# Performance work log

Hardware: AMD Instinct MI355X
Metric: run time of the kernel (lower is better)

The kernel has to match this reference:

```python
import jax, jax.numpy as jnp
import numpy as np

B, N, DIN, DH = 16, 512, 128, 256
NEG = -9.0e15  # matches -9000000000000000.0 in torch source


def _xavier(key, fan_in, fan_out):
    lim = float(np.sqrt(6.0 / (fan_in + fan_out)))
    return jax.random.uniform(key, (fan_in, fan_out), jnp.float32, -lim, lim)


def _l2n(x, eps=1e-12):
    # torch F.normalize: x / max(||x||, eps)
    return x / jnp.maximum(jnp.linalg.norm(x, axis=-1, keepdims=True), eps)


def _prelu(x, a):
    return jnp.where(x >= 0, x, a * x)


def setup_inputs() -> dict:
    key = jax.random.key(0)
    ks = jax.random.split(key, 12)
    seq = jax.random.normal(ks[0], (B, N, DIN), jnp.float32)
    # sparse-ish nonnegative adjacency with self loops, row-normalized
    u = jax.random.uniform(ks[1], (B, N, N), jnp.float32)
    a = jnp.where(u < 0.1, u, 0.0) + jnp.eye(N, dtype=jnp.float32)[None]
    adj = a / a.sum(-1, keepdims=True)
    # dense diffusion matrix, row-normalized
    d = jax.random.uniform(ks[2], (B, N, N), jnp.float32)
    diff = d / d.sum(-1, keepdims=True)
    # dropout keep-mask for F.dropout(p=0.1, training=True)
    keep = jax.random.bernoulli(ks[3], 0.9, (B, N, N)).astype(jnp.float32)
    drop_mask = keep / 0.9
    return {
        "seq": seq, "adj": adj, "diff": diff, "drop_mask": drop_mask,
        "fc1_w": _xavier(ks[4], DIN, DH),
        "q_w": _xavier(ks[5], DH, DH),
        "k_w": _xavier(ks[6], DH, DH),
        "v_w1": _xavier(ks[7], DH, DH),
        "v_w2": _xavier(ks[8], DH, DH),
        "fc2_w": _xavier(ks[9], DIN, DH),
        "bias1": jnp.zeros((DH,), jnp.float32),
        "bias2": jnp.zeros((DH,), jnp.float32),
        "prelu1_a": jnp.float32(0.25),
        "prelu2_a": jnp.float32(0.25),
        "v_prelu_a": jnp.float32(0.25),
    }


def reference(seq, adj, diff, drop_mask, fc1_w, q_w, k_w, v_w1, v_w2,
              fc2_w, bias1, bias2, prelu1_a, prelu2_a, v_prelu_a):
    # ---- GCN1 (attention branch) ----
    fts = seq @ fc1_w                                   # [B,N,H]
    out = jnp.einsum('bmn,bnh->bmh', adj, fts)          # adj aggregation
    q = _l2n(out @ q_w)
    k = _l2n(out @ k_w)
    scores = jax.lax.stop_gradient(jnp.einsum('bmd,bnd->bmn', q, k))  # .detach()
    div_loss = jnp.mean(jnp.sum((q - k) ** 2, axis=-1))
    att = jnp.where(adj > 0, scores, NEG)
    att = jax.nn.softmax(att, axis=-1) * drop_mask      # dropout(p=0.1)
    agg = jnp.einsum('bmn,bnh->bmh', att, out)
    v = _prelu(agg @ v_w1, v_prelu_a) @ v_w2 + bias1
    h1 = _prelu(v, prelu1_a)
    # ---- GCN2 (plain branch) ----
    h2 = _prelu(jnp.einsum('bmn,bnh->bmh', diff, seq @ fc2_w) + bias2, prelu2_a)
    # ---- Readout ----
    c1 = jnp.mean(h1, axis=1)                           # [B,H]
    c2 = jnp.mean(h2, axis=1)
    # ---- DIS ----
    n1 = _l2n(h1).reshape(B * N, DH)
    n2 = _l2n(h2).reshape(B * N, DH)
    node_logits = n1 @ n2.T                             # [B*N, B*N]
    graph_logits = _l2n(c1) @ _l2n(c2).T                # [B, B]
    return node_logits, graph_logits, div_loss
```

## Files before the change

kernel.cpp:

```cpp
#include <hip/hip_runtime.h>
#include <hip/hip_bf16.h>


using bf16x8 = __attribute__((ext_vector_type(8))) short;
using f32x4  = __attribute__((ext_vector_type(4))) float;

__device__ __forceinline__ unsigned short f2b(float f) {
    union { float f; unsigned int u; } x; x.f = f;
    unsigned int r = x.u + 0x7FFFu + ((x.u >> 16) & 1u);
    return (unsigned short)(r >> 16);
}
__device__ __forceinline__ float b2f(unsigned short u) {
    union { unsigned int u; float f; } x; x.u = (unsigned int)u << 16;
    return x.f;
}
__device__ __forceinline__ void gload_lds16(const void* g, void* l) {
    __builtin_amdgcn_global_load_lds(
        (const __attribute__((address_space(1))) void*)g,
        (__attribute__((address_space(3))) void*)l, 16, 0, 0);
}

__global__ __launch_bounds__(256) void conv3(const float* __restrict__ seq,
                                             const float* __restrict__ adj,
                                             const float* __restrict__ diff,
                                             unsigned short* __restrict__ seq_bf,
                                             unsigned short* __restrict__ adj_bf,
                                             unsigned short* __restrict__ diff_bf) {
    long i = (long)blockIdx.x * 256 + threadIdx.x;
    const float* src; unsigned short* dst; long off;
    if (i < 262144)       { src = seq;  dst = seq_bf;  off = i; }
    else if (i < 1310720) { src = adj;  dst = adj_bf;  off = i - 262144; }
    else                  { src = diff; dst = diff_bf; off = i - 1310720; }
    float4 v = reinterpret_cast<const float4*>(src)[off];
    ushort4 o; o.x = f2b(v.x); o.y = f2b(v.y); o.z = f2b(v.z); o.w = f2b(v.w);
    reinterpret_cast<ushort4*>(dst)[off] = o;
}

__global__ void wtrans6(const float* __restrict__ fc1, const float* __restrict__ fc2,
                        const float* __restrict__ qw,  const float* __restrict__ kw,
                        const float* __restrict__ v1,  const float* __restrict__ v2,
                        unsigned short* fc1T, unsigned short* fc2T,
                        unsigned short* qwT,  unsigned short* kwT,
                        unsigned short* v1T,  unsigned short* v2T) {
    __shared__ float t[32][33];
    const int z = blockIdx.z;
    const float* in; unsigned short* op; int R;
    const int C = 256;
    if      (z == 0) { in = fc1; op = fc1T; R = 128; }
    else if (z == 1) { in = fc2; op = fc2T; R = 128; }
    else if (z == 2) { in = qw;  op = qwT;  R = 256; }
    else if (z == 3) { in = kw;  op = kwT;  R = 256; }
    else if (z == 4) { in = v1;  op = v1T;  R = 256; }
    else             { in = v2;  op = v2T;  R = 256; }
    int c0 = blockIdx.x * 32, r0 = blockIdx.y * 32;
    if (r0 >= R) return;
    int x = threadIdx.x, y = threadIdx.y;
    for (int i = 0; i < 32; i += 8) t[y + i][x] = in[(long)(r0 + y + i) * C + c0 + x];
    __syncthreads();
    for (int i = 0; i < 32; i += 8)
        op[(long)(c0 + y + i) * R + r0 + x] = f2b(t[x][y + i]);
}

#define BN 128
#define BK 64

template<int TBM, int EPI, bool WF, bool WB, bool WT, bool SWZ>
__global__ __launch_bounds__(256) void gemm_nt(
    const unsigned short* __restrict__ A, const unsigned short* __restrict__ Bt,
    float* __restrict__ Cf, unsigned short* __restrict__ Cb, unsigned short* __restrict__ Ct,
    int M, int Nn, int K, int lda, int ldb, int ldc, int ldt,
    long sA, long sB, long sC, long sT,
    const float* __restrict__ bias, const float* __restrict__ alpha_ptr)
{
    constexpr int MI = TBM / 32;
    __shared__ unsigned short As[TBM][BK];
    __shared__ unsigned short Bs[BN][BK];
    const int b = blockIdx.z;
    A  += (long)b * sA;
    Bt += (long)b * sB;
    const long cbase = (long)b * sC;
    const long tbase = (long)b * sT;

    int tx, ty;
    if (SWZ) {
        int bid = blockIdx.y * gridDim.x + blockIdx.x;
        int nwg = gridDim.x * gridDim.y;
        int cpx = nwg >> 3;
        int s = (bid & 7) * cpx + (bid >> 3);
        tx = s % gridDim.x; ty = s / gridDim.x;
    } else { tx = blockIdx.x; ty = blockIdx.y; }
    const int tile_m = ty * TBM;
    const int tile_n = tx * BN;

    const int tid  = threadIdx.x;
    const int lane = tid & 63;
    const int wave = tid >> 6;
    const int wm = (wave >> 1) * (TBM / 2);
    const int wn = (wave & 1) << 6;
    const int lrow = lane >> 3;
    const int lcol = (lane & 7) << 3;

    f32x4 acc[MI][4] = {};

    for (int k0 = 0; k0 < K; k0 += BK) {
        #pragma unroll
        for (int i = 0; i < TBM / 32; ++i) {
            const int rb = (i * 4 + wave) * 8;
            gload_lds16(A + (long)(tile_m + rb + lrow) * lda + k0 + lcol, &As[rb][0]);
        }
        #pragma unroll
        for (int i = 0; i < 4; ++i) {
            const int rb = (i * 4 + wave) * 8;
            gload_lds16(Bt + (long)(tile_n + rb + lrow) * ldb + k0 + lcol, &Bs[rb][0]);
        }
        __syncthreads();
        #pragma unroll
        for (int ks = 0; ks < 2; ++ks) {
            const int kk = ks * 32 + ((lane >> 4) << 3);
            bf16x8 af[MI], bq[4];
            #pragma unroll
            for (int mi = 0; mi < MI; ++mi)
                af[mi] = *reinterpret_cast<const bf16x8*>(&As[wm + (lane & 15) + mi * 16][kk]);
            #pragma unroll
            for (int ni = 0; ni < 4; ++ni)
                bq[ni] = *reinterpret_cast<const bf16x8*>(&Bs[wn + (lane & 15) + ni * 16][kk]);
            #pragma unroll
            for (int mi = 0; mi < MI; ++mi)
                #pragma unroll
                for (int ni = 0; ni < 4; ++ni)
                    acc[mi][ni] = __builtin_amdgcn_mfma_f32_16x16x32_bf16(
                        af[mi], bq[ni], acc[mi][ni], 0, 0, 0);
        }
        __syncthreads();
    }

    const float alpha = (EPI & 1) ? alpha_ptr[0] : 0.f;
    const int c0 = lane & 15;
    const int r0 = (lane >> 4) << 2;
    #pragma unroll
    for (int ni = 0; ni < 4; ++ni) {
        const int col = tile_n + wn + ni * 16 + c0;
        const float bv = (EPI & 2) ? bias[col] : 0.f;
        #pragma unroll
        for (int mi = 0; mi < MI; ++mi) {
            const int row0 = tile_m + wm + mi * 16 + r0;
            float v[4];
            #pragma unroll
            for (int j = 0; j < 4; ++j) {
                float x = acc[mi][ni][j] + bv;
                if (EPI & 1) x = (x >= 0.f) ? x : alpha * x;
                v[j] = x;
            }
            if (WF) {
                #pragma unroll
                for (int j = 0; j < 4; ++j)
                    Cf[cbase + (long)(row0 + j) * ldc + col] = v[j];
            }
            if (WB) {
                #pragma unroll
                for (int j = 0; j < 4; ++j)
                    Cb[cbase + (long)(row0 + j) * ldc + col] = f2b(v[j]);
            }
            if (WT) {
                ushort4 o; o.x = f2b(v[0]); o.y = f2b(v[1]); o.z = f2b(v[2]); o.w = f2b(v[3]);
                *reinterpret_cast<ushort4*>(&Ct[tbase + (long)col * ldt + row0]) = o;
            }
        }
    }
}

__global__ __launch_bounds__(256) void gemm_norm(
    const unsigned short* __restrict__ A, const unsigned short* __restrict__ Bt,
    unsigned short* __restrict__ n_out, float* __restrict__ psum,
    const float* __restrict__ bias, const float* __restrict__ alpha_ptr,
    int K, int lda, int ldb, long sA, long sB)
{
    __shared__ unsigned short As[32][BK];
    __shared__ unsigned short Bs[256][BK];
    __shared__ float rowred[32][4];
    A  += (long)blockIdx.z * sA;
    Bt += (long)blockIdx.z * sB;
    const int p = blockIdx.z * gridDim.y + blockIdx.y;
    const int arow0 = blockIdx.y * 32;
    const long grow0 = (long)p * 32;

    const int tid  = threadIdx.x;
    const int lane = tid & 63;
    const int wave = tid >> 6;
    const int wn = wave << 6;
    const int lrow = lane >> 3;
    const int lcol = (lane & 7) << 3;

    f32x4 acc[2][4] = {};

    for (int k0 = 0; k0 < K; k0 += BK) {
        {
            const int rb = wave * 8;
            gload_lds16(A + (long)(arow0 + rb + lrow) * lda + k0 + lcol, &As[rb][0]);
        }
        #pragma unroll
        for (int i = 0; i < 8; ++i) {
            const int rb = (i * 4 + wave) * 8;
            gload_lds16(Bt + (long)(rb + lrow) * ldb + k0 + lcol, &Bs[rb][0]);
        }
        __syncthreads();
        #pragma unroll
        for (int ks = 0; ks < 2; ++ks) {
            const int kk = ks * 32 + ((lane >> 4) << 3);
            bf16x8 af[2], bq[4];
            #pragma unroll
            for (int mi = 0; mi < 2; ++mi)
                af[mi] = *reinterpret_cast<const bf16x8*>(&As[(lane & 15) + mi * 16][kk]);
            #pragma unroll
            for (int ni = 0; ni < 4; ++ni)
                bq[ni] = *reinterpret_cast<const bf16x8*>(&Bs[wn + (lane & 15) + ni * 16][kk]);
            #pragma unroll
            for (int mi = 0; mi < 2; ++mi)
                #pragma unroll
                for (int ni = 0; ni < 4; ++ni)
                    acc[mi][ni] = __builtin_amdgcn_mfma_f32_16x16x32_bf16(
                        af[mi], bq[ni], acc[mi][ni], 0, 0, 0);
        }
        __syncthreads();
    }

    const float alpha = alpha_ptr[0];
    const int c0 = lane & 15;
    const int r0 = (lane >> 4) << 2;
    float rs[2][4] = {};
    #pragma unroll
    for (int ni = 0; ni < 4; ++ni) {
        const float bv = bias[wn + ni * 16 + c0];
        #pragma unroll
        for (int mi = 0; mi < 2; ++mi)
            #pragma unroll
            for (int j = 0; j < 4; ++j) {
                float x = acc[mi][ni][j] + bv;
                x = (x >= 0.f) ? x : alpha * x;
                acc[mi][ni][j] = x;
                rs[mi][j] += x * x;
            }
    }
    #pragma unroll
    for (int o = 1; o <= 8; o <<= 1)
        #pragma unroll
        for (int mi = 0; mi < 2; ++mi)
            #pragma unroll
            for (int j = 0; j < 4; ++j) rs[mi][j] += __shfl_xor(rs[mi][j], o);
    if ((lane & 15) == 0) {
        #pragma unroll
        for (int mi = 0; mi < 2; ++mi)
            #pragma unroll
            for (int j = 0; j < 4; ++j) rowred[mi * 16 + r0 + j][wave] = rs[mi][j];
    }
    __syncthreads();
    float inv[2][4];
    #pragma unroll
    for (int mi = 0; mi < 2; ++mi)
        #pragma unroll
        for (int j = 0; j < 4; ++j) {
            const int r = mi * 16 + r0 + j;
            float s = rowred[r][0] + rowred[r][1] + rowred[r][2] + rowred[r][3];
            inv[mi][j] = 1.f / fmaxf(sqrtf(s), 1e-12f);
        }
    float cs[4];
    #pragma unroll
    for (int ni = 0; ni < 4; ++ni) {
        float s = 0.f;
        #pragma unroll
        for (int mi = 0; mi < 2; ++mi)
            #pragma unroll
            for (int j = 0; j < 4; ++j) s += acc[mi][ni][j];
        s += __shfl_xor(s, 16);
        s += __shfl_xor(s, 32);
        cs[ni] = s;
    }
    if (lane < 16) {
        #pragma unroll
        for (int ni = 0; ni < 4; ++ni)
            psum[(long)p * 256 + wn + ni * 16 + lane] = cs[ni];
    }
    #pragma unroll
    for (int ni = 0; ni < 4; ++ni)
        #pragma unroll
        for (int mi = 0; mi < 2; ++mi)
            #pragma unroll
            for (int j = 0; j < 4; ++j)
                n_out[(grow0 + mi * 16 + r0 + j) * 256 + wn + ni * 16 + c0] =
                    f2b(acc[mi][ni][j] * inv[mi][j]);
}

__global__ __launch_bounds__(256) void qk_post(const float* __restrict__ qk,
                                               unsigned short* __restrict__ q_bf,
                                               unsigned short* __restrict__ k_bf,
                                               float* __restrict__ rowpart) {
    long row = blockIdx.x; int t = threadIdx.x;
    float v = qk[row * 512 + t];
    float w = qk[row * 512 + 256 + t];
    float sq = v * v, sk = w * w;
    #pragma unroll
    for (int o = 32; o; o >>= 1) { sq += __shfl_xor(sq, o); sk += __shfl_xor(sk, o); }
    __shared__ float rq[4], rk[4], rd[4];
    if ((t & 63) == 0) { rq[t >> 6] = sq; rk[t >> 6] = sk; }
    __syncthreads();
    sq = rq[0] + rq[1] + rq[2] + rq[3];
    sk = rk[0] + rk[1] + rk[2] + rk[3];
    float qn = v / fmaxf(sqrtf(sq), 1e-12f);
    float kn = w / fmaxf(sqrtf(sk), 1e-12f);
    q_bf[row * 256 + t] = f2b(qn);
    k_bf[row * 256 + t] = f2b(kn);
    float d = qn - kn, sd = d * d;
    #pragma unroll
    for (int o = 32; o; o >>= 1) sd += __shfl_xor(sd, o);
    if ((t & 63) == 0) rd[t >> 6] = sd;
    __syncthreads();
    if (t == 0) rowpart[row] = rd[0] + rd[1] + rd[2] + rd[3];
}

__global__ __launch_bounds__(256) void att_softmax(const unsigned short* __restrict__ scores,
                                                   const unsigned short* __restrict__ adj_bf,
                                                   const float* __restrict__ drop,
                                                   unsigned short* __restrict__ att) {
    long base = ((long)blockIdx.y * 512 + blockIdx.x) * 512;
    int t = threadIdx.x;
    unsigned short a0 = adj_bf[base + t], a1 = adj_bf[base + t + 256];
    float s0 = b2f(scores[base + t]), s1 = b2f(scores[base + t + 256]);
    bool m0 = a0 != 0, m1 = a1 != 0;
    float mx = fmaxf(m0 ? s0 : -1e30f, m1 ? s1 : -1e30f);
    #pragma unroll
    for (int o = 32; o; o >>= 1) mx = fmaxf(mx, __shfl_xor(mx, o));
    __shared__ float redm[4], reds[4];
    if ((t & 63) == 0) redm[t >> 6] = mx;
    __syncthreads();
    mx = fmaxf(fmaxf(redm[0], redm[1]), fmaxf(redm[2], redm[3]));
    float e0 = m0 ? __expf(s0 - mx) : 0.f;
    float e1 = m1 ? __expf(s1 - mx) : 0.f;
    float sm = e0 + e1;
    #pragma unroll
    for (int o = 32; o; o >>= 1) sm += __shfl_xor(sm, o);
    if ((t & 63) == 0) reds[t >> 6] = sm;
    __syncthreads();
    sm = reds[0] + reds[1] + reds[2] + reds[3];
    float inv = 1.f / sm;
    att[base + t]       = f2b(e0 * inv * drop[base + t]);
    att[base + t + 256] = f2b(e1 * inv * drop[base + t + 256]);
}

__global__ __launch_bounds__(256) void graphf2(const float* __restrict__ psum1,
                                               const float* __restrict__ psum2,
                                               const float* __restrict__ rowpart,
                                               float* __restrict__ out_g,
                                               float* __restrict__ out_div) {
    __shared__ float a[16][256], bsm[16][256];
    int t = threadIdx.x, g = t >> 4, l = t & 15;
    float va[16], vb[16]; float s1 = 0.f, s2 = 0.f;
    #pragma unroll
    for (int i = 0; i < 16; ++i) {
        const int col = l + i * 16;
        float m1 = 0.f, m2 = 0.f;
        for (int c = 0; c < 16; ++c) {
            m1 += psum1[(long)(g * 16 + c) * 256 + col];
            m2 += psum2[(long)(g * 16 + c) * 256 + col];
        }
        va[i] = m1 * (1.f / 512.f); s1 += va[i] * va[i];
        vb[i] = m2 * (1.f / 512.f); s2 += vb[i] * vb[i];
    }
    #pragma unroll
    for (int o = 8; o; o >>= 1) { s1 += __shfl_xor(s1, o, 16); s2 += __shfl_xor(s2, o, 16); }
    float d1 = fmaxf(sqrtf(s1), 1e-12f), d2 = fmaxf(sqrtf(s2), 1e-12f);
    #pragma unroll
    for (int i = 0; i < 16; ++i) {
        a[g][l + i * 16] = va[i] / d1;
        bsm[g][l + i * 16] = vb[i] / d2;
    }
    __syncthreads();
    int ii = t >> 4, jj = t & 15;
    float s = 0.f;
    for (int h = 0; h < 256; ++h) s += a[ii][h] * bsm[jj][h];
    out_g[ii * 16 + jj] = s;
    float ds = 0.f;
    for (int i = t; i < 8192; i += 256) ds += rowpart[i];
    #pragma unroll
    for (int o = 32; o; o >>= 1) ds += __shfl_xor(ds, o);
    __shared__ float red[4];
    if ((t & 63) == 0) red[t >> 6] = ds;
    __syncthreads();
    if (t == 0) out_div[0] = (red[0] + red[1] + red[2] + red[3]) * (1.f / 8192.f);
}

static constexpr long OFF_SEQ_BF  = 0;
static constexpr long OFF_FC1T    = 2097152;
static constexpr long OFF_FC2T    = OFF_FC1T + 65536;
static constexpr long OFF_QWT     = OFF_FC2T + 65536;
static constexpr long OFF_KWT     = OFF_QWT + 131072;
static constexpr long OFF_VW1T    = OFF_KWT + 131072;
static constexpr long OFF_VW2T    = OFF_VW1T + 131072;
static constexpr long OFF_ROWPART = OFF_VW2T + 131072;
static constexpr long OFF_ADJATT  = 3145728;
static constexpr long OFF_DIFFBF  = OFF_ADJATT + 8388608;
static constexpr long OFF_FTST    = OFF_DIFFBF + 8388608;
static constexpr long OFF_OUTT    = OFF_FTST + 4194304;
static constexpr long OFF_QF      = OFF_OUTT + 4194304;
static constexpr long OFF_QBF     = OFF_QF + 16777216;
static constexpr long OFF_KBF     = OFF_QBF + 4194304;
static constexpr long OFF_SCORES  = OFF_KBF + 4194304;

extern "C" void kernel_launch(void* const* d_in, const int* in_sizes, int n_in,
                              void* d_out, int out_size, void* d_ws, size_t ws_size,
                              hipStream_t stream) {
    const float* seq      = (const float*)d_in[0];
    const float* adj      = (const float*)d_in[1];
    const float* diff     = (const float*)d_in[2];
    const float* drop     = (const float*)d_in[3];
    const float* fc1_w    = (const float*)d_in[4];
    const float* q_w      = (const float*)d_in[5];
    const float* k_w      = (const float*)d_in[6];
    const float* v_w1     = (const float*)d_in[7];
    const float* v_w2     = (const float*)d_in[8];
    const float* fc2_w    = (const float*)d_in[9];
    const float* bias1    = (const float*)d_in[10];
    const float* bias2    = (const float*)d_in[11];
    const float* prelu1_a = (const float*)d_in[12];
    const float* prelu2_a = (const float*)d_in[13];
    const float* v_prelu  = (const float*)d_in[14];
    float* out = (float*)d_out;

    char* ws = (char*)d_ws;
    unsigned short* seq_bf  = (unsigned short*)(ws + OFF_SEQ_BF);
    unsigned short* fc1T    = (unsigned short*)(ws + OFF_FC1T);
    unsigned short* fc2T    = (unsigned short*)(ws + OFF_FC2T);
    unsigned short* qwT     = (unsigned short*)(ws + OFF_QWT);
    unsigned short* kwT     = (unsigned short*)(ws + OFF_KWT);
    unsigned short* vw1T    = (unsigned short*)(ws + OFF_VW1T);
    unsigned short* vw2T    = (unsigned short*)(ws + OFF_VW2T);
    float*          rowpart = (float*)(ws + OFF_ROWPART);
    unsigned short* adj_bf  = (unsigned short*)(ws + OFF_ADJATT);
    unsigned short* att_bf  = (unsigned short*)(ws + OFF_ADJATT);
    unsigned short* diff_bf = (unsigned short*)(ws + OFF_DIFFBF);
    unsigned short* ftsT    = (unsigned short*)(ws + OFF_FTST);
    unsigned short* outT    = (unsigned short*)(ws + OFF_OUTT);
    float*          qk_f    = (float*)(ws + OFF_QF);
    float*          psum1   = (float*)(ws + OFF_QF);
    float*          psum2   = (float*)(ws + OFF_QF + 262144);
    unsigned short* q_bf    = (unsigned short*)(ws + OFF_QBF);
    unsigned short* agg_bf  = (unsigned short*)(ws + OFF_QBF);
    unsigned short* fts2T   = (unsigned short*)(ws + OFF_QBF);
    unsigned short* k_bf    = (unsigned short*)(ws + OFF_KBF);
    unsigned short* t1_bf   = (unsigned short*)(ws + OFF_KBF);
    unsigned short* out_bf  = (unsigned short*)(ws + OFF_SCORES);
    unsigned short* scoresb = (unsigned short*)(ws + OFF_SCORES);
    unsigned short* n1_bf   = (unsigned short*)(ws + OFF_SCORES);
    unsigned short* n2_bf   = (unsigned short*)(ws + OFF_SCORES + 4194304);

    conv3<<<9216, 256, 0, stream>>>(seq, adj, diff, seq_bf, adj_bf, diff_bf);
    wtrans6<<<dim3(8, 8, 6), dim3(32, 8), 0, stream>>>(
        fc1_w, fc2_w, q_w, k_w, v_w1, v_w2, fc1T, fc2T, qwT, kwT, vw1T, vw2T);

    gemm_nt<64, 0, false, true, false, false><<<dim3(64, 4, 1), 256, 0, stream>>>(
        fc1T, seq_bf, nullptr, ftsT, nullptr,
        256, 8192, 128, 128, 128, 8192, 0, 0, 0, 0, 0, nullptr, nullptr);

    gemm_nt<64, 0, false, true, true, false><<<dim3(2, 8, 16), 256, 0, stream>>>(
        adj_bf, ftsT, nullptr, out_bf, outT,
        512, 256, 512, 512, 8192, 256, 512, 262144, 512, 131072, 131072, nullptr, nullptr);

    gemm_nt<128, 0, true, false, false, false><<<dim3(4, 64, 1), 256, 0, stream>>>(
        out_bf, qwT, qk_f, nullptr, nullptr,
        8192, 512, 256, 256, 256, 512, 0, 0, 0, 0, 0, nullptr, nullptr);

    qk_post<<<8192, 256, 0, stream>>>(qk_f, q_bf, k_bf, rowpart);

    gemm_nt<64, 0, false, true, false, false><<<dim3(4, 8, 16), 256, 0, stream>>>(
        q_bf, k_bf, nullptr, scoresb, nullptr,
        512, 512, 256, 256, 256, 512, 0, 131072, 131072, 262144, 0, nullptr, nullptr);

    att_softmax<<<dim3(512, 16), 256, 0, stream>>>(scoresb, adj_bf, drop, att_bf);

    gemm_nt<64, 0, false, true, false, false><<<dim3(2, 8, 16), 256, 0, stream>>>(
        att_bf, outT, nullptr, agg_bf, nullptr,
        512, 256, 512, 512, 512, 256, 0, 262144, 131072, 131072, 0, nullptr, nullptr);

    gemm_nt<64, 1, false, true, false, false><<<dim3(2, 128, 1), 256, 0, stream>>>(
        agg_bf, vw1T, nullptr, t1_bf, nullptr,
        8192, 256, 256, 256, 256, 256, 0, 0, 0, 0, 0, nullptr, v_prelu);

    gemm_norm<<<dim3(1, 256, 1), 256, 0, stream>>>(
        t1_bf, vw2T, n1_bf, psum1, bias1, prelu1_a, 256, 256, 256, 0, 0);

    gemm_nt<64, 0, false, true, false, false><<<dim3(64, 4, 1), 256, 0, stream>>>(
        fc2T, seq_bf, nullptr, fts2T, nullptr,
        256, 8192, 128, 128, 128, 8192, 0, 0, 0, 0, 0, nullptr, nullptr);

    gemm_norm<<<dim3(1, 16, 16), 256, 0, stream>>>(
        diff_bf, fts2T, n2_bf, psum2, bias2, prelu2_a, 512, 512, 8192, 262144, 512);

    graphf2<<<1, 256, 0, stream>>>(psum1, psum2, rowpart, out + 67108864, out + 67109120);

    gemm_nt<128, 0, true, false, false, true><<<dim3(64, 64, 1), 256, 0, stream>>>(
        n1_bf, n2_bf, out, nullptr, nullptr,
        8192, 8192, 256, 256, 256, 8192, 0, 0, 0, 0, 0, nullptr, nullptr);

    (void)in_sizes; (void)n_in; (void)out_size; (void)ws_size;
}
```

Measured before the change: 239.8 us.

## Fuse attention chain, QK projection with normalization, and two-layer MLP into single kernels

```diff
diff --git a/kernel.cpp b/kernel.cpp
--- a/kernel.cpp
+++ b/kernel.cpp
@@ -9,10 +9,6 @@
     union { float f; unsigned int u; } x; x.f = f;
     unsigned int r = x.u + 0x7FFFu + ((x.u >> 16) & 1u);
     return (unsigned short)(r >> 16);
-}
-__device__ __forceinline__ float b2f(unsigned short u) {
-    union { unsigned int u; float f; } x; x.u = (unsigned int)u << 16;
-    return x.f;
 }
 __device__ __forceinline__ void gload_lds16(const void* g, void* l) {
     __builtin_amdgcn_global_load_lds(
@@ -290,93 +286,464 @@
                     f2b(acc[mi][ni][j] * inv[mi][j]);
 }
 
-__global__ __launch_bounds__(256) void qk_post(const float* __restrict__ qk,
-                                               unsigned short* __restrict__ q_bf,
-                                               unsigned short* __restrict__ k_bf,
-                                               float* __restrict__ rowpart) {
-    long row = blockIdx.x; int t = threadIdx.x;
-    float v = qk[row * 512 + t];
-    float w = qk[row * 512 + 256 + t];
-    float sq = v * v, sk = w * w;
-    #pragma unroll
-    for (int o = 32; o; o >>= 1) { sq += __shfl_xor(sq, o); sk += __shfl_xor(sk, o); }
-    __shared__ float rq[4], rk[4], rd[4];
-    if ((t & 63) == 0) { rq[t >> 6] = sq; rk[t >> 6] = sk; }
-    __syncthreads();
-    sq = rq[0] + rq[1] + rq[2] + rq[3];
-    sk = rk[0] + rk[1] + rk[2] + rk[3];
-    float qn = v / fmaxf(sqrtf(sq), 1e-12f);
-    float kn = w / fmaxf(sqrtf(sk), 1e-12f);
-    q_bf[row * 256 + t] = f2b(qn);
-    k_bf[row * 256 + t] = f2b(kn);
-    float d = qn - kn, sd = d * d;
-    #pragma unroll
-    for (int o = 32; o; o >>= 1) sd += __shfl_xor(sd, o);
-    if ((t & 63) == 0) rd[t >> 6] = sd;
-    __syncthreads();
-    if (t == 0) rowpart[row] = rd[0] + rd[1] + rd[2] + rd[3];
-}
-
-__global__ __launch_bounds__(256) void att_softmax(const unsigned short* __restrict__ scores,
-                                                   const unsigned short* __restrict__ adj_bf,
-                                                   const float* __restrict__ drop,
-                                                   unsigned short* __restrict__ att) {
-    long base = ((long)blockIdx.y * 512 + blockIdx.x) * 512;
-    int t = threadIdx.x;
-    unsigned short a0 = adj_bf[base + t], a1 = adj_bf[base + t + 256];
-    float s0 = b2f(scores[base + t]), s1 = b2f(scores[base + t + 256]);
-    bool m0 = a0 != 0, m1 = a1 != 0;
-    float mx = fmaxf(m0 ? s0 : -1e30f, m1 ? s1 : -1e30f);
-    #pragma unroll
-    for (int o = 32; o; o >>= 1) mx = fmaxf(mx, __shfl_xor(mx, o));
-    __shared__ float redm[4], reds[4];
-    if ((t & 63) == 0) redm[t >> 6] = mx;
-    __syncthreads();
-    mx = fmaxf(fmaxf(redm[0], redm[1]), fmaxf(redm[2], redm[3]));
-    float e0 = m0 ? __expf(s0 - mx) : 0.f;
-    float e1 = m1 ? __expf(s1 - mx) : 0.f;
-    float sm = e0 + e1;
-    #pragma unroll
-    for (int o = 32; o; o >>= 1) sm += __shfl_xor(sm, o);
-    if ((t & 63) == 0) reds[t >> 6] = sm;
-    __syncthreads();
-    sm = reds[0] + reds[1] + reds[2] + reds[3];
-    float inv = 1.f / sm;
-    att[base + t]       = f2b(e0 * inv * drop[base + t]);
-    att[base + t + 256] = f2b(e1 * inv * drop[base + t + 256]);
-}
-
-__global__ __launch_bounds__(256) void graphf2(const float* __restrict__ psum1,
+__global__ __launch_bounds__(256) void qk_proj(
+    const unsigned short* __restrict__ outb,
+    const unsigned short* __restrict__ qkT,
+    unsigned short* __restrict__ q_bf,
+    unsigned short* __restrict__ k_bf)
+{
+    __shared__ unsigned short As[32 * 64];
+    __shared__ unsigned short Bs[512 * 64];
+    __shared__ float sred[32][4];
+    const long m0 = (long)blockIdx.x * 32;
+    const int tid = threadIdx.x, lane = tid & 63, wave = tid >> 6;
+    const int lrow = lane >> 3, lcol = (lane & 7) << 3;
+    const int hi = lane >> 4, c0 = lane & 15, r0 = hi << 2;
+    const int wn = wave << 7;
+
+    f32x4 acc[2][8] = {};
+    for (int k0 = 0; k0 < 256; k0 += 64) {
+        gload_lds16(outb + (m0 + wave * 8 + lrow) * 256 + k0 + lcol, &As[wave * 8 * 64]);
+        #pragma unroll
+        for (int i = 0; i < 16; ++i) {
+            const int rb = (i * 4 + wave) * 8;
+            gload_lds16(qkT + (long)(rb + lrow) * 256 + k0 + lcol, &Bs[rb * 64]);
+        }
+        __syncthreads();
+        #pragma unroll
+        for (int ks = 0; ks < 2; ++ks) {
+            const int kk = ks * 32 + (hi << 3);
+            bf16x8 af[2], bq[8];
+            #pragma unroll
+            for (int mi = 0; mi < 2; ++mi)
+                af[mi] = *reinterpret_cast<const bf16x8*>(&As[(mi * 16 + c0) * 64 + kk]);
+            #pragma unroll
+            for (int ni = 0; ni < 8; ++ni)
+                bq[ni] = *reinterpret_cast<const bf16x8*>(&Bs[(wn + ni * 16 + c0) * 64 + kk]);
+            #pragma unroll
+            for (int mi = 0; mi < 2; ++mi)
+                #pragma unroll
+                for (int ni = 0; ni < 8; ++ni)
+                    acc[mi][ni] = __builtin_amdgcn_mfma_f32_16x16x32_bf16(
+                        af[mi], bq[ni], acc[mi][ni], 0, 0, 0);
+        }
+        __syncthreads();
+    }
+    float rs[2][4] = {};
+    #pragma unroll
+    for (int mi = 0; mi < 2; ++mi)
+        #pragma unroll
+        for (int ni = 0; ni < 8; ++ni)
+            #pragma unroll
+            for (int j = 0; j < 4; ++j) { float x = acc[mi][ni][j]; rs[mi][j] += x * x; }
+    #pragma unroll
+    for (int o = 1; o <= 8; o <<= 1)
+        #pragma unroll
+        for (int mi = 0; mi < 2; ++mi)
+            #pragma unroll
+            for (int j = 0; j < 4; ++j) rs[mi][j] += __shfl_xor(rs[mi][j], o);
+    if (c0 == 0) {
+        #pragma unroll
+        for (int mi = 0; mi < 2; ++mi)
+            #pragma unroll
+            for (int j = 0; j < 4; ++j) sred[mi * 16 + r0 + j][wave] = rs[mi][j];
+    }
+    __syncthreads();
+    float inv[2][4];
+    #pragma unroll
+    for (int mi = 0; mi < 2; ++mi)
+        #pragma unroll
+        for (int j = 0; j < 4; ++j) {
+            const int r = mi * 16 + r0 + j;
+            float sq = sred[r][0] + sred[r][1];
+            float sk = sred[r][2] + sred[r][3];
+            inv[mi][j] = 1.f / fmaxf(sqrtf(wave < 2 ? sq : sk), 1e-12f);
+        }
+    #pragma unroll
+    for (int mi = 0; mi < 2; ++mi)
+        #pragma unroll
+        for (int ni = 0; ni < 8; ++ni)
+            #pragma unroll
+            for (int j = 0; j < 4; ++j) {
+                const long rowg = m0 + mi * 16 + r0 + j;
+                const int col = wn + ni * 16 + c0;
+                unsigned short v = f2b(acc[mi][ni][j] * inv[mi][j]);
+                if (wave < 2) q_bf[rowg * 256 + col] = v;
+                else          k_bf[rowg * 256 + col - 256] = v;
+            }
+}
+
+__global__ __launch_bounds__(256) void att_fused(
+    const unsigned short* __restrict__ q_bf,
+    const unsigned short* __restrict__ k_bf,
+    const unsigned short* __restrict__ adj_bf,
+    const float* __restrict__ drop,
+    const unsigned short* __restrict__ outT,
+    unsigned short* __restrict__ agg_bf,
+    float* __restrict__ rowpart)
+{
+    __shared__ unsigned char smem[69632];
+    unsigned short* As  = (unsigned short*)smem;
+    unsigned short* Bs  = (unsigned short*)(smem + 4096);
+    unsigned short* Pls = (unsigned short*)smem;
+    unsigned short* Bs2 = (unsigned short*)(smem + 34816);
+    __shared__ float redm[32][4], reds[32][4];
+
+    const int b  = blockIdx.y;
+    const int m0 = blockIdx.x << 5;
+    const unsigned short* qp = q_bf + (long)b * 131072 + (long)m0 * 256;
+    const unsigned short* kp = k_bf + (long)b * 131072;
+    const unsigned short* ot = outT + (long)b * 131072;
+    const unsigned short* ap = adj_bf + ((long)b * 512 + m0) * 512;
+    const float*          dp = drop   + ((long)b * 512 + m0) * 512;
+
+    const int tid = threadIdx.x, lane = tid & 63, wave = tid >> 6;
+    const int lrow = lane >> 3, lcol = (lane & 7) << 3;
+    const int hi = lane >> 4, c0 = lane & 15, r0 = hi << 2;
+    const int wn = wave << 7;
+
+    f32x4 acc[2][8] = {};
+    for (int k0 = 0; k0 < 256; k0 += 64) {
+        gload_lds16(qp + (long)(wave * 8 + lrow) * 256 + k0 + lcol, &As[wave * 8 * 64]);
+        #pragma unroll
+        for (int i = 0; i < 16; ++i) {
+            const int rb = (i * 4 + wave) * 8;
+            gload_lds16(kp + (long)(rb + lrow) * 256 + k0 + lcol, &Bs[rb * 64]);
+        }
+        __syncthreads();
+        #pragma unroll
+        for (int ks = 0; ks < 2; ++ks) {
+            const int kk = ks * 32 + (hi << 3);
+            bf16x8 af[2], bq[8];
+            #pragma unroll
+            for (int mi = 0; mi < 2; ++mi)
+                af[mi] = *reinterpret_cast<const bf16x8*>(&As[(mi * 16 + c0) * 64 + kk]);
+            #pragma unroll
+            for (int ni = 0; ni < 8; ++ni)
+                bq[ni] = *reinterpret_cast<const bf16x8*>(&Bs[(wn + ni * 16 + c0) * 64 + kk]);
+            #pragma unroll
+            for (int mi = 0; mi < 2; ++mi)
+                #pragma unroll
+                for (int ni = 0; ni < 8; ++ni)
+                    acc[mi][ni] = __builtin_amdgcn_mfma_f32_16x16x32_bf16(
+                        af[mi], bq[ni], acc[mi][ni], 0, 0, 0);
+        }
+        __syncthreads();
+    }
+
+    float rmax[2][4];
+    #pragma unroll
+    for (int mi = 0; mi < 2; ++mi)
+        #pragma unroll
+        for (int j = 0; j < 4; ++j) rmax[mi][j] = -3.0e38f;
+    #pragma unroll
+    for (int mi = 0; mi < 2; ++mi)
+        #pragma unroll
+        for (int ni = 0; ni < 8; ++ni)
+            #pragma unroll
+            for (int j = 0; j < 4; ++j) {
+                const int rowl = mi * 16 + r0 + j;
+                const int col  = wn + ni * 16 + c0;
+                float s = acc[mi][ni][j];
+                if (col == m0 + rowl)
+                    rowpart[(long)b * 512 + m0 + rowl] = 2.f - 2.f * s;
+                bool m = ap[(long)rowl * 512 + col] != 0;
+                s = m ? s : -3.0e38f;
+                acc[mi][ni][j] = s;
+                rmax[mi][j] = fmaxf(rmax[mi][j], s);
+            }
+    #pragma unroll
+    for (int o = 1; o <= 8; o <<= 1)
+        #pragma unroll
+        for (int mi = 0; mi < 2; ++mi)
+            #pragma unroll
+            for (int j = 0; j < 4; ++j) rmax[mi][j] = fmaxf(rmax[mi][j], __shfl_xor(rmax[mi][j], o));
+    if (c0 == 0) {
+        #pragma unroll
+        for (int mi = 0; mi < 2; ++mi)
+            #pragma unroll
+            for (int j = 0; j < 4; ++j) redm[mi * 16 + r0 + j][wave] = rmax[mi][j];
+    }
+    __syncthreads();
+    float mx[2][4], rsum[2][4];
+    #pragma unroll
+    for (int mi = 0; mi < 2; ++mi)
+        #pragma unroll
+        for (int j = 0; j < 4; ++j) {
+            const int r = mi * 16 + r0 + j;
+            mx[mi][j] = fmaxf(fmaxf(redm[r][0], redm[r][1]), fmaxf(redm[r][2], redm[r][3]));
+            rsum[mi][j] = 0.f;
+        }
+    #pragma unroll
+    for (int mi = 0; mi < 2; ++mi)
+        #pragma unroll
+        for (int ni = 0; ni < 8; ++ni)
+            #pragma unroll
+            for (int j = 0; j < 4; ++j) {
+                float e = __expf(acc[mi][ni][j] - mx[mi][j]);
+                acc[mi][ni][j] = e;
+                rsum[mi][j] += e;
+            }
+    #pragma unroll
+    for (int o = 1; o <= 8; o <<= 1)
+        #pragma unroll
+        for (int mi = 0; mi < 2; ++mi)
+            #pragma unroll
+            for (int j = 0; j < 4; ++j) rsum[mi][j] += __shfl_xor(rsum[mi][j], o);
+    if (c0 == 0) {
+        #pragma unroll
+        for (int mi = 0; mi < 2; ++mi)
+            #pragma unroll
+            for (int j = 0; j < 4; ++j) reds[mi * 16 + r0 + j][wave] = rsum[mi][j];
+    }
+    __syncthreads();
+    float inv[2][4];
+    #pragma unroll
+    for (int mi = 0; mi < 2; ++mi)
+        #pragma unroll
+        for (int j = 0; j < 4; ++j) {
+            const int r = mi * 16 + r0 + j;
+            inv[mi][j] = 1.f / (reds[r][0] + reds[r][1] + reds[r][2] + reds[r][3]);
+        }
+    #pragma unroll
+    for (int mi = 0; mi < 2; ++mi)
+        #pragma unroll
+        for (int ni = 0; ni < 8; ++ni)
+            #pragma unroll
+            for (int j = 0; j < 4; ++j) {
+                const int rowl = mi * 16 + r0 + j;
+                const int col  = wn + ni * 16 + c0;
+                float p = acc[mi][ni][j] * inv[mi][j] * dp[(long)rowl * 512 + col];
+                Pls[rowl * 520 + col] = f2b(p);
+            }
+    __syncthreads();
+
+    f32x4 acc2[2][4] = {};
+    for (int k0 = 0; k0 < 512; k0 += 64) {
+        #pragma unroll
+        for (int i = 0; i < 8; ++i) {
+            const int rb = (i * 4 + wave) * 8;
+            gload_lds16(ot + (long)(rb + lrow) * 512 + k0 + lcol, &Bs2[rb * 64]);
+        }
+        __syncthreads();
+        #pragma unroll
+        for (int ks = 0; ks < 2; ++ks) {
+            const int kk = ks * 32 + (hi << 3);
+            bf16x8 af[2], bq[4];
+            #pragma unroll
+            for (int mi = 0; mi < 2; ++mi)
+                af[mi] = *reinterpret_cast<const bf16x8*>(&Pls[(mi * 16 + c0) * 520 + k0 + kk]);
+            #pragma unroll
+            for (int ni = 0; ni < 4; ++ni)
+                bq[ni] = *reinterpret_cast<const bf16x8*>(&Bs2[((wave << 6) + ni * 16 + c0) * 64 + kk]);
+            #pragma unroll
+            for (int mi = 0; mi < 2; ++mi)
+                #pragma unroll
+                for (int ni = 0; ni < 4; ++ni)
+                    acc2[mi][ni] = __builtin_amdgcn_mfma_f32_16x16x32_bf16(
+                        af[mi], bq[ni], acc2[mi][ni], 0, 0, 0);
+        }
+        __syncthreads();
+    }
+    #pragma unroll
+    for (int mi = 0; mi < 2; ++mi)
+        #pragma unroll
+        for (int ni = 0; ni < 4; ++ni)
+            #pragma unroll
+            for (int j = 0; j < 4; ++j) {
+                const int rowl = mi * 16 + r0 + j;
+                const int col  = (wave << 6) + ni * 16 + c0;
+                agg_bf[((long)b * 512 + m0 + rowl) * 256 + col] = f2b(acc2[mi][ni][j]);
+            }
+}
+
+__global__ __launch_bounds__(256) void mlp_norm(
+    const unsigned short* __restrict__ agg,
+    const unsigned short* __restrict__ w1T,
+    const unsigned short* __restrict__ w2T,
+    const float* __restrict__ bias,
+    const float* __restrict__ av, const float* __restrict__ a1,
+    unsigned short* __restrict__ n_out,
+    float* __restrict__ psum)
+{
+    __shared__ unsigned char smem[49664];
+    unsigned short* As  = (unsigned short*)smem;
+    unsigned short* Bs  = (unsigned short*)(smem + 4096);
+    unsigned short* T   = (unsigned short*)smem;
+    unsigned short* Bs2 = (unsigned short*)(smem + 16896);
+    __shared__ float rowred[32][4];
+
+    const int p = blockIdx.x;
+    const long row0 = (long)p * 32;
+    const int tid = threadIdx.x, lane = tid & 63, wave = tid >> 6;
+    const int lrow = lane >> 3, lcol = (lane & 7) << 3;
+    const int hi = lane >> 4, c0 = lane & 15, r0 = hi << 2;
+    const int wn = wave << 6;
+
+    f32x4 acc[2][4] = {};
+    for (int k0 = 0; k0 < 256; k0 += 64) {
+        gload_lds16(agg + (row0 + wave * 8 + lrow) * 256 + k0 + lcol, &As[wave * 8 * 64]);
+        #pragma unroll
+        for (int i = 0; i < 8; ++i) {
+            const int rb = (i * 4 + wave) * 8;
+            gload_lds16(w1T + (long)(rb + lrow) * 256 + k0 + lcol, &Bs[rb * 64]);
+        }
+        __syncthreads();
+        #pragma unroll
+        for (int ks = 0; ks < 2; ++ks) {
+            const int kk = ks * 32 + (hi << 3);
+            bf16x8 af[2], bq[4];
+            #pragma unroll
+            for (int mi = 0; mi < 2; ++mi)
+                af[mi] = *reinterpret_cast<const bf16x8*>(&As[(mi * 16 + c0) * 64 + kk]);
+            #pragma unroll
+            for (int ni = 0; ni < 4; ++ni)
+                bq[ni] = *reinterpret_cast<const bf16x8*>(&Bs[(wn + ni * 16 + c0) * 64 + kk]);
+            #pragma unroll
+            for (int mi = 0; mi < 2; ++mi)
+                #pragma unroll
+                for (int ni = 0; ni < 4; ++ni)
+                    acc[mi][ni] = __builtin_amdgcn_mfma_f32_16x16x32_bf16(
+                        af[mi], bq[ni], acc[mi][ni], 0, 0, 0);
+        }
+        __syncthreads();
+    }
+    const float alphav = av[0];
+    #pragma unroll
+    for (int mi = 0; mi < 2; ++mi)
+        #pragma unroll
+        for (int ni = 0; ni < 4; ++ni)
+            #pragma unroll
+            for (int j = 0; j < 4; ++j) {
+                const int rowl = mi * 16 + r0 + j;
+                const int col  = wn + ni * 16 + c0;
+                float x = acc[mi][ni][j];
+                x = (x >= 0.f) ? x : alphav * x;
+                T[rowl * 264 + col] = f2b(x);
+            }
+    __syncthreads();
+
+    f32x4 acc2[2][4] = {};
+    for (int k0 = 0; k0 < 256; k0 += 64) {
+        #pragma unroll
+        for (int i = 0; i < 8; ++i) {
+            const int rb = (i * 4 + wave) * 8;
+            gload_lds16(w2T + (long)(rb + lrow) * 256 + k0 + lcol, &Bs2[rb * 64]);
+        }
+        __syncthreads();
+        #pragma unroll
+        for (int ks = 0; ks < 2; ++ks) {
+            const int kk = ks * 32 + (hi << 3);
+            bf16x8 af[2], bq[4];
+            #pragma unroll
+            for (int mi = 0; mi < 2; ++mi)
+                af[mi] = *reinterpret_cast<const bf16x8*>(&T[(mi * 16 + c0) * 264 + k0 + kk]);
+            #pragma unroll
+            for (int ni = 0; ni < 4; ++ni)
+                bq[ni] = *reinterpret_cast<const bf16x8*>(&Bs2[(wn + ni * 16 + c0) * 64 + kk]);
+            #pragma unroll
+            for (int mi = 0; mi < 2; ++mi)
+                #pragma unroll
+                for (int ni = 0; ni < 4; ++ni)
+                    acc2[mi][ni] = __builtin_amdgcn_mfma_f32_16x16x32_bf16(
+                        af[mi], bq[ni], acc2[mi][ni], 0, 0, 0);
+        }
+        __syncthreads();
+    }
+    const float alpha1 = a1[0];
+    float rs[2][4] = {};
+    #pragma unroll
+    for (int ni = 0; ni < 4; ++ni) {
+        const float bv = bias[wn + ni * 16 + c0];
+        #pragma unroll
+        for (int mi = 0; mi < 2; ++mi)
+            #pragma unroll
+            for (int j = 0; j < 4; ++j) {
+                float x = acc2[mi][ni][j] + bv;
+                x = (x >= 0.f) ? x : alpha1 * x;
+                acc2[mi][ni][j] = x;
+                rs[mi][j] += x * x;
+            }
+    }
+    #pragma unroll
+    for (int o = 1; o <= 8; o <<= 1)
+        #pragma unroll
+        for (int mi = 0; mi < 2; ++mi)
+            #pragma unroll
+            for (int j = 0; j < 4; ++j) rs[mi][j] += __shfl_xor(rs[mi][j], o);
+    if (c0 == 0) {
+        #pragma unroll
+        for (int mi = 0; mi < 2; ++mi)
+            #pragma unroll
+            for (int j = 0; j < 4; ++j) rowred[mi * 16 + r0 + j][wave] = rs[mi][j];
+    }
+    __syncthreads();
+    float inv[2][4];
+    #pragma unroll
+    for (int mi = 0; mi < 2; ++mi)
+        #pragma unroll
+        for (int j = 0; j < 4; ++j) {
+            const int r = mi * 16 + r0 + j;
+            float s = rowred[r][0] + rowred[r][1] + rowred[r][2] + rowred[r][3];
+            inv[mi][j] = 1.f / fmaxf(sqrtf(s), 1e-12f);
+        }
+    float cs[4];
+    #pragma unroll
+    for (int ni = 0; ni < 4; ++ni) {
+        float s = 0.f;
+        #pragma unroll
+        for (int mi = 0; mi < 2; ++mi)
+            #pragma unroll
+            for (int j = 0; j < 4; ++j) s += acc2[mi][ni][j];
+        s += __shfl_xor(s, 16);
+        s += __shfl_xor(s, 32);
+        cs[ni] = s;
+    }
+    if (lane < 16) {
+        #pragma unroll
+        for (int ni = 0; ni < 4; ++ni)
+            psum[(long)p * 256 + wn + ni * 16 + lane] = cs[ni];
+    }
+    #pragma unroll
+    for (int mi = 0; mi < 2; ++mi)
+        #pragma unroll
+        for (int ni = 0; ni < 4; ++ni)
+            #pragma unroll
+            for (int j = 0; j < 4; ++j)
+                n_out[(row0 + mi * 16 + r0 + j) * 256 + wn + ni * 16 + c0] =
+                    f2b(acc2[mi][ni][j] * inv[mi][j]);
+}
+
+__global__ __launch_bounds__(256) void creduce(const float* __restrict__ psum1,
                                                const float* __restrict__ psum2,
+                                               float* __restrict__ c1n,
+                                               float* __restrict__ c2n) {
+    const int which = blockIdx.x & 1, g = blockIdx.x >> 1;
+    const float* ps = which ? psum2 : psum1;
+    float* cn = which ? c2n : c1n;
+    const int t = threadIdx.x;
+    float s = 0.f;
+    #pragma unroll
+    for (int c = 0; c < 16; ++c) s += ps[(long)(g * 16 + c) * 256 + t];
+    s *= (1.f / 512.f);
+    float ss = s * s;
+    #pragma unroll
+    for (int o = 32; o; o >>= 1) ss += __shfl_xor(ss, o);
+    __shared__ float red[4];
+    if ((t & 63) == 0) red[t >> 6] = ss;
+    __syncthreads();
+    float tot = red[0] + red[1] + red[2] + red[3];
+    cn[g * 256 + t] = s / fmaxf(sqrtf(tot), 1e-12f);
+}
+
+__global__ __launch_bounds__(256) void graphf3(const float* __restrict__ c1n,
+                                               const float* __restrict__ c2n,
                                                const float* __restrict__ rowpart,
                                                float* __restrict__ out_g,
                                                float* __restrict__ out_div) {
-    __shared__ float a[16][256], bsm[16][256];
-    int t = threadIdx.x, g = t >> 4, l = t & 15;
-    float va[16], vb[16]; float s1 = 0.f, s2 = 0.f;
-    #pragma unroll
-    for (int i = 0; i < 16; ++i) {
-        const int col = l + i * 16;
-        float m1 = 0.f, m2 = 0.f;
-        for (int c = 0; c < 16; ++c) {
-            m1 += psum1[(long)(g * 16 + c) * 256 + col];
-            m2 += psum2[(long)(g * 16 + c) * 256 + col];
-        }
-        va[i] = m1 * (1.f / 512.f); s1 += va[i] * va[i];
-        vb[i] = m2 * (1.f / 512.f); s2 += vb[i] * vb[i];
-    }
-    #pragma unroll
-    for (int o = 8; o; o >>= 1) { s1 += __shfl_xor(s1, o, 16); s2 += __shfl_xor(s2, o, 16); }
-    float d1 = fmaxf(sqrtf(s1), 1e-12f), d2 = fmaxf(sqrtf(s2), 1e-12f);
-    #pragma unroll
-    for (int i = 0; i < 16; ++i) {
-        a[g][l + i * 16] = va[i] / d1;
-        bsm[g][l + i * 16] = vb[i] / d2;
-    }
-    __syncthreads();
-    int ii = t >> 4, jj = t & 15;
+    const int t = threadIdx.x, ii = t >> 4, jj = t & 15;
     float s = 0.f;
-    for (int h = 0; h < 256; ++h) s += a[ii][h] * bsm[jj][h];
+    for (int h = 0; h < 256; ++h) s += c1n[ii * 256 + h] * c2n[jj * 256 + h];
     out_g[ii * 16 + jj] = s;
     float ds = 0.f;
     for (int i = t; i < 8192; i += 256) ds += rowpart[i];
@@ -390,20 +757,23 @@
 
 static constexpr long OFF_SEQ_BF  = 0;
 static constexpr long OFF_FC1T    = 2097152;
-static constexpr long OFF_FC2T    = OFF_FC1T + 65536;
-static constexpr long OFF_QWT     = OFF_FC2T + 65536;
-static constexpr long OFF_KWT     = OFF_QWT + 131072;
-static constexpr long OFF_VW1T    = OFF_KWT + 131072;
-static constexpr long OFF_VW2T    = OFF_VW1T + 131072;
-static constexpr long OFF_ROWPART = OFF_VW2T + 131072;
-static constexpr long OFF_ADJATT  = 3145728;
-static constexpr long OFF_DIFFBF  = OFF_ADJATT + 8388608;
-static constexpr long OFF_FTST    = OFF_DIFFBF + 8388608;
-static constexpr long OFF_OUTT    = OFF_FTST + 4194304;
-static constexpr long OFF_QF      = OFF_OUTT + 4194304;
-static constexpr long OFF_QBF     = OFF_QF + 16777216;
-static constexpr long OFF_KBF     = OFF_QBF + 4194304;
-static constexpr long OFF_SCORES  = OFF_KBF + 4194304;
+static constexpr long OFF_QWT     = 2228224;
+static constexpr long OFF_VW1T    = 2490368;
+static constexpr long OFF_VW2T    = 2621440;
+static constexpr long OFF_ROWPART = 2752512;
+static constexpr long OFF_C1N     = 2785280;
+static constexpr long OFF_C2N     = 2801664;
+static constexpr long OFF_ADJ     = 3145728;
+static constexpr long OFF_DIFF    = 11534336;
+static constexpr long OFF_FTST    = 19922944;
+static constexpr long OFF_OUTT    = 28311552;
+static constexpr long OFF_OUTBF   = 32505856;
+static constexpr long OFF_QBF     = 36700160;
+static constexpr long OFF_KBF     = 40894464;
+static constexpr long OFF_AGG     = 45088768;
+static constexpr long OFF_PSUM    = 49283072;
+static constexpr long OFF_N1      = 49807360;
+static constexpr long OFF_N2      = 54001664;
 
 extern "C" void kernel_launch(void* const* d_in, const int* in_sizes, int n_in,
                               void* d_out, int out_size, void* d_ws, size_t ws_size,
@@ -428,73 +798,53 @@
     char* ws = (char*)d_ws;
     unsigned short* seq_bf  = (unsigned short*)(ws + OFF_SEQ_BF);
     unsigned short* fc1T    = (unsigned short*)(ws + OFF_FC1T);
-    unsigned short* fc2T    = (unsigned short*)(ws + OFF_FC2T);
+    unsigned short* fc2T    = (unsigned short*)(ws + OFF_FC1T + 65536);
     unsigned short* qwT     = (unsigned short*)(ws + OFF_QWT);
-    unsigned short* kwT     = (unsigned short*)(ws + OFF_KWT);
+    unsigned short* kwT     = (unsigned short*)(ws + OFF_QWT + 131072);
     unsigned short* vw1T    = (unsigned short*)(ws + OFF_VW1T);
     unsigned short* vw2T    = (unsigned short*)(ws + OFF_VW2T);
     float*          rowpart = (float*)(ws + OFF_ROWPART);
-    unsigned short* adj_bf  = (unsigned short*)(ws + OFF_ADJATT);
-    unsigned short* att_bf  = (unsigned short*)(ws + OFF_ADJATT);
-    unsigned short* diff_bf = (unsigned short*)(ws + OFF_DIFFBF);
+    float*          c1n     = (float*)(ws + OFF_C1N);
+    float*          c2n     = (float*)(ws + OFF_C2N);
+    unsigned short* adj_bf  = (unsigned short*)(ws + OFF_ADJ);
+    unsigned short* diff_bf = (unsigned short*)(ws + OFF_DIFF);
     unsigned short* ftsT    = (unsigned short*)(ws + OFF_FTST);
+    unsigned short* fts2T   = (unsigned short*)(ws + OFF_FTST + 4194304);
     unsigned short* outT    = (unsigned short*)(ws + OFF_OUTT);
-    float*          qk_f    = (float*)(ws + OFF_QF);
-    float*          psum1   = (float*)(ws + OFF_QF);
-    float*          psum2   = (float*)(ws + OFF_QF + 262144);
+    unsigned short* out_bf  = (unsigned short*)(ws + OFF_OUTBF);
     unsigned short* q_bf    = (unsigned short*)(ws + OFF_QBF);
-    unsigned short* agg_bf  = (unsigned short*)(ws + OFF_QBF);
-    unsigned short* fts2T   = (unsigned short*)(ws + OFF_QBF);
     unsigned short* k_bf    = (unsigned short*)(ws + OFF_KBF);
-    unsigned short* t1_bf   = (unsigned short*)(ws + OFF_KBF);
-    unsigned short* out_bf  = (unsigned short*)(ws + OFF_SCORES);
-    unsigned short* scoresb = (unsigned short*)(ws + OFF_SCORES);
-    unsigned short* n1_bf   = (unsigned short*)(ws + OFF_SCORES);
-    unsigned short* n2_bf   = (unsigned short*)(ws + OFF_SCORES + 4194304);
+    unsigned short* agg_bf  = (unsigned short*)(ws + OFF_AGG);
+    float*          psum1   = (float*)(ws + OFF_PSUM);
+    float*          psum2   = (float*)(ws + OFF_PSUM + 262144);
+    unsigned short* n1_bf   = (unsigned short*)(ws + OFF_N1);
+    unsigned short* n2_bf   = (unsigned short*)(ws + OFF_N2);
 
     conv3<<<9216, 256, 0, stream>>>(seq, adj, diff, seq_bf, adj_bf, diff_bf);
     wtrans6<<<dim3(8, 8, 6), dim3(32, 8), 0, stream>>>(
         fc1_w, fc2_w, q_w, k_w, v_w1, v_w2, fc1T, fc2T, qwT, kwT, vw1T, vw2T);
 
-    gemm_nt<64, 0, false, true, false, false><<<dim3(64, 4, 1), 256, 0, stream>>>(
+    gemm_nt<64, 0, false, true, false, false><<<dim3(64, 4, 2), 256, 0, stream>>>(
         fc1T, seq_bf, nullptr, ftsT, nullptr,
-        256, 8192, 128, 128, 128, 8192, 0, 0, 0, 0, 0, nullptr, nullptr);
+        256, 8192, 128, 128, 128, 8192, 0, 32768, 0, 2097152, 0, nullptr, nullptr);
 
     gemm_nt<64, 0, false, true, true, false><<<dim3(2, 8, 16), 256, 0, stream>>>(
         adj_bf, ftsT, nullptr, out_bf, outT,
         512, 256, 512, 512, 8192, 256, 512, 262144, 512, 131072, 131072, nullptr, nullptr);
 
-    gemm_nt<128, 0, true, false, false, false><<<dim3(4, 64, 1), 256, 0, stream>>>(
-        out_bf, qwT, qk_f, nullptr, nullptr,
-        8192, 512, 256, 256, 256, 512, 0, 0, 0, 0, 0, nullptr, nullptr);
-
-    qk_post<<<8192, 256, 0, stream>>>(qk_f, q_bf, k_bf, rowpart);
-
-    gemm_nt<64, 0, false, true, false, false><<<dim3(4, 8, 16), 256, 0, stream>>>(
-        q_bf, k_bf, nullptr, scoresb, nullptr,
-        512, 512, 256, 256, 256, 512, 0, 131072, 131072, 262144, 0, nullptr, nullptr);
-
-    att_softmax<<<dim3(512, 16), 256, 0, stream>>>(scoresb, adj_bf, drop, att_bf);
-
-    gemm_nt<64, 0, false, true, false, false><<<dim3(2, 8, 16), 256, 0, stream>>>(
-        att_bf, outT, nullptr, agg_bf, nullptr,
-        512, 256, 512, 512, 512, 256, 0, 262144, 131072, 131072, 0, nullptr, nullptr);
-
-    gemm_nt<64, 1, false, true, false, false><<<dim3(2, 128, 1), 256, 0, stream>>>(
-        agg_bf, vw1T, nullptr, t1_bf, nullptr,
-        8192, 256, 256, 256, 256, 256, 0, 0, 0, 0, 0, nullptr, v_prelu);
-
-    gemm_norm<<<dim3(1, 256, 1), 256, 0, stream>>>(
-        t1_bf, vw2T, n1_bf, psum1, bias1, prelu1_a, 256, 256, 256, 0, 0);
-
-    gemm_nt<64, 0, false, true, false, false><<<dim3(64, 4, 1), 256, 0, stream>>>(
-        fc2T, seq_bf, nullptr, fts2T, nullptr,
-        256, 8192, 128, 128, 128, 8192, 0, 0, 0, 0, 0, nullptr, nullptr);
-
     gemm_norm<<<dim3(1, 16, 16), 256, 0, stream>>>(
         diff_bf, fts2T, n2_bf, psum2, bias2, prelu2_a, 512, 512, 8192, 262144, 512);
 
-    graphf2<<<1, 256, 0, stream>>>(psum1, psum2, rowpart, out + 67108864, out + 67109120);
+    qk_proj<<<256, 256, 0, stream>>>(out_bf, qwT, q_bf, k_bf);
+
+    att_fused<<<dim3(16, 16), 256, 0, stream>>>(
+        q_bf, k_bf, adj_bf, drop, outT, agg_bf, rowpart);
+
+    mlp_norm<<<256, 256, 0, stream>>>(
+        agg_bf, vw1T, vw2T, bias1, v_prelu, prelu1_a, n1_bf, psum1);
+
+    creduce<<<32, 256, 0, stream>>>(psum1, psum2, c1n, c2n);
+    graphf3<<<1, 256, 0, stream>>>(c1n, c2n, rowpart, out + 67108864, out + 67109120);
 
     gemm_nt<128, 0, true, false, false, true><<<dim3(64, 64, 1), 256, 0, stream>>>(
         n1_bf, n2_bf, out, nullptr, nullptr,
```

Result: faster. 209.3 us (-12.7%).
